# Kernel tuning notes

Hardware: AMD Instinct MI355X
Metric: run time of the kernel (lower is better)

## Reference

```python
import jax, jax.numpy as jnp
import numpy as np

SCALE = 2
K_UP = 5
K_ENC = 3
EPS = 1e-5


def _conv(x, w, b, pad):
    y = jax.lax.conv_general_dilated(x, w, (1, 1), [(pad, pad), (pad, pad)],
                                     dimension_numbers=('NCHW', 'OIHW', 'NCHW'))
    return y + b[None, :, None, None]


def _bn(x, g, b, m, v):
    return g[None, :, None, None] * (x - m[None, :, None, None]) * jax.lax.rsqrt(v[None, :, None, None] + EPS) + b[None, :, None, None]


def _pixel_shuffle(x, r):
    b, c, h, w = x.shape
    co = c // (r * r)
    return x.reshape(b, co, r, r, h, w).transpose(0, 1, 4, 2, 5, 3).reshape(b, co, h * r, w * r)


def setup_inputs() -> dict:
    key = jax.random.key(0)
    ks = jax.random.split(key, 8)
    c, c_mid = 256, 64
    k_enc_out = (SCALE * K_UP) ** 2  # 100
    inp = {
        'X': jax.random.normal(ks[0], (8, c, 64, 64), dtype=jnp.float32),
        'comp_w': jax.random.normal(ks[1], (c_mid, c, 1, 1), dtype=jnp.float32) * (2.0 / c) ** 0.5,
        'comp_b': jnp.zeros((c_mid,), jnp.float32),
        'bn1_g': jnp.ones((c_mid,), jnp.float32),
        'bn1_b': jnp.zeros((c_mid,), jnp.float32),
        'bn1_m': jnp.zeros((c_mid,), jnp.float32),
        'bn1_v': jnp.ones((c_mid,), jnp.float32),
        'enc_w': jax.random.normal(ks[2], (k_enc_out, c_mid, K_ENC, K_ENC), dtype=jnp.float32) * (2.0 / (c_mid * K_ENC * K_ENC)) ** 0.5,
        'enc_b': jnp.zeros((k_enc_out,), jnp.float32),
        'bn2_g': jnp.ones((k_enc_out,), jnp.float32),
        'bn2_b': jnp.zeros((k_enc_out,), jnp.float32),
        'bn2_m': jnp.zeros((k_enc_out,), jnp.float32),
        'bn2_v': jnp.ones((k_enc_out,), jnp.float32),
    }
    return inp


def reference(X, comp_w, comp_b, bn1_g, bn1_b, bn1_m, bn1_v,
              enc_w, enc_b, bn2_g, bn2_b, bn2_m, bn2_v):
    b, c, h, w = X.shape
    h_, w_ = h * SCALE, w * SCALE
    # kernel prediction branch
    W = jax.nn.relu(_bn(_conv(X, comp_w, comp_b, 0), bn1_g, bn1_b, bn1_m, bn1_v))
    W = _bn(_conv(W, enc_w, enc_b, K_ENC // 2), bn2_g, bn2_b, bn2_m, bn2_v)
    W = _pixel_shuffle(W, SCALE)            # (b, k_up^2, h_, w_)
    W = jax.nn.softmax(W, axis=1)
    # content branch: bilinear upsample (align_corners=False / half-pixel)
    Xu = jax.image.resize(X, (b, c, h_, w_), method='bilinear')
    pad = (K_UP // 2) * SCALE               # = 4
    Xp = jnp.pad(Xu, ((0, 0), (0, 0), (pad, pad), (pad, pad)))
    # fused unfold (dilation=SCALE) + softmax-weighted reassembly
    out = jnp.zeros((b, c, h_, w_), X.dtype)
    k = 0
    for i in range(K_UP):
        for j in range(K_UP):
            patch = jax.lax.dynamic_slice(Xp, (0, 0, i * SCALE, j * SCALE), (b, c, h_, w_))
            out = out + W[:, k, None] * patch
            k += 1
    return out
```

## Files before the change

kernel.cpp:

```cpp
#include <hip/hip_runtime.h>

#define EPS 1e-5f

__global__ void k0_prep(const float* __restrict__ comp_w, const float* __restrict__ comp_b,
                        const float* __restrict__ bn1_g, const float* __restrict__ bn1_b,
                        const float* __restrict__ bn1_m, const float* __restrict__ bn1_v,
                        const float* __restrict__ enc_w, const float* __restrict__ enc_b,
                        const float* __restrict__ bn2_g, const float* __restrict__ bn2_b,
                        const float* __restrict__ bn2_m, const float* __restrict__ bn2_v,
                        float* __restrict__ W1wT, float* __restrict__ b1f,
                        float* __restrict__ encT, float* __restrict__ biasT)
{
    int gtid = blockIdx.x * 256 + threadIdx.x;
    int gstride = gridDim.x * 256;
    for (int i = gtid; i < 256 * 64; i += gstride) {
        int cin = i >> 6, co = i & 63;
        float s = bn1_g[co] * rsqrtf(bn1_v[co] + EPS);
        W1wT[i] = comp_w[co * 256 + cin] * s;
    }
    for (int i = gtid; i < 64; i += gstride) {
        float s = bn1_g[i] * rsqrtf(bn1_v[i] + EPS);
        b1f[i] = (comp_b[i] - bn1_m[i]) * s + bn1_b[i];
    }
    for (int i = gtid; i < 4 * 64 * 9 * 32; i += gstride) {
        int k = i & 31;
        int rest = i >> 5;
        int dxy = rest % 9;
        int tmp = rest / 9;
        int cin = tmp & 63, p = tmp >> 6;
        float v = 0.f;
        if (k < 25) {
            int ko = 4 * k + p;
            float s = bn2_g[ko] * rsqrtf(bn2_v[ko] + EPS);
            v = enc_w[(ko * 64 + cin) * 9 + dxy] * s;
        }
        encT[i] = v;
    }
    for (int i = gtid; i < 4 * 32; i += gstride) {
        int p = i >> 5, k = i & 31;
        float v = 0.f;
        if (k < 25) {
            int ko = 4 * k + p;
            float s = bn2_g[ko] * rsqrtf(bn2_v[ko] + EPS);
            v = (enc_b[ko] - bn2_m[ko]) * s + bn2_b[ko];
        }
        biasT[i] = v;
    }
}

__global__ __launch_bounds__(256, 4) void k1_conv1(const float* __restrict__ X,
                                                   const float* __restrict__ W1wT,
                                                   const float* __restrict__ b1f,
                                                   float* __restrict__ W1)
{
    int blk = blockIdx.x;
    int b   = blk >> 5;
    int pt  = blk & 31;
    int tid = threadIdx.x;
    int coh  = __builtin_amdgcn_readfirstlane(tid >> 7);
    int posl = tid & 127;
    int pos  = pt * 128 + posl;
    const float* xp = X + (size_t)b * 256 * 4096 + pos;
    const float* wp = W1wT + coh * 32;
    float acc[32];
#pragma unroll
    for (int k = 0; k < 32; ++k) acc[k] = 0.f;
#pragma unroll 8
    for (int cin = 0; cin < 256; ++cin) {
        float x = xp[(size_t)cin * 4096];
        const float* w = wp + cin * 64;
#pragma unroll
        for (int k = 0; k < 32; ++k) acc[k] = fmaf(w[k], x, acc[k]);
    }
    float* op = W1 + ((size_t)b * 64 + coh * 32) * 4096 + pos;
#pragma unroll
    for (int k = 0; k < 32; ++k) {
        float v = acc[k] + b1f[coh * 32 + k];
        op[(size_t)k * 4096] = fmaxf(v, 0.f);
    }
}

__global__ __launch_bounds__(512, 4) void k2_conv2(const float* __restrict__ W1,
                                                   const float* __restrict__ encT,
                                                   const float* __restrict__ biasT,
                                                   float* __restrict__ Wsm)
{
    __shared__ float tile[6400];
    __shared__ float red[6400];
    int blk = blockIdx.x;
    int tc = blk & 7;
    int tr = (blk >> 3) & 7;
    int b  = blk >> 6;
    int tid = threadIdx.x;

    const float* wb = W1 + (size_t)b * 64 * 4096;
    for (int i = tid; i < 6400; i += 512) {
        int cin = i / 100;
        int rr = (i - cin * 100) / 10;
        int cc = i - cin * 100 - rr * 10;
        int r = tr * 8 - 1 + rr, c = tc * 8 - 1 + cc;
        float v = 0.f;
        if (r >= 0 && r < 64 && c >= 0 && c < 64) v = wb[cin * 4096 + r * 64 + c];
        tile[i] = v;
    }
    __syncthreads();

    int w    = tid >> 6;
    int p    = __builtin_amdgcn_readfirstlane(w & 3);
    int cinh = __builtin_amdgcn_readfirstlane(w >> 2);
    int lane = tid & 63;
    int pr = lane >> 3, pc = lane & 7;
    const float* wt = encT + (size_t)(p * 576 + cinh * 288) * 32;
    const float* tp = tile + cinh * 32 * 100;
    float acc[25];
#pragma unroll
    for (int k = 0; k < 25; ++k) acc[k] = 0.f;

    for (int cin = 0; cin < 32; ++cin) {
#pragma unroll
        for (int dy = 0; dy < 3; ++dy) {
#pragma unroll
            for (int dx = 0; dx < 3; ++dx) {
                float v = tp[cin * 100 + (pr + dy) * 10 + (pc + dx)];
                const float* wv = wt + (cin * 9 + dy * 3 + dx) * 32;
#pragma unroll
                for (int k = 0; k < 25; ++k) acc[k] = fmaf(wv[k], v, acc[k]);
            }
        }
    }

    if (cinh == 0) {
        float* rp = red + (p * 64 + lane) * 25;
#pragma unroll
        for (int k = 0; k < 25; ++k) rp[k] = acc[k];
    }
    __syncthreads();
    if (cinh == 1) {
        const float* rp = red + (p * 64 + lane) * 25;
#pragma unroll
        for (int k = 0; k < 25; ++k) acc[k] += rp[k];

        const float* bp = biasT + p * 32;
        float mx = -1e30f;
#pragma unroll
        for (int k = 0; k < 25; ++k) { acc[k] += bp[k]; mx = fmaxf(mx, acc[k]); }
        float sum = 0.f;
#pragma unroll
        for (int k = 0; k < 25; ++k) { acc[k] = __expf(acc[k] - mx); sum += acc[k]; }
        float rs = 1.f / sum;
#pragma unroll
        for (int k = 0; k < 25; ++k) acc[k] *= rs;

        int py = p >> 1, px = p & 1;
        int y = (tr * 8 + pr) * 2 + py, x = (tc * 8 + pc) * 2 + px;
        float* op = Wsm + (((size_t)b * 128 + y) * 128 + x) * 28;
#pragma unroll
        for (int k = 0; k < 6; ++k) {
            float4 v = make_float4(acc[k*4], acc[k*4+1], acc[k*4+2], acc[k*4+3]);
            *(float4*)(op + k * 4) = v;
        }
        op[24] = acc[24];
    }
}

#define LOADW(W, q) do { \
    float4 t0 = *(const float4*)(q);       float4 t1 = *(const float4*)((q) + 4);  \
    float4 t2 = *(const float4*)((q) + 8); float4 t3 = *(const float4*)((q) + 12); \
    float4 t4 = *(const float4*)((q) + 16); float4 t5 = *(const float4*)((q) + 20); \
    W[0]=t0.x; W[1]=t0.y; W[2]=t0.z; W[3]=t0.w; \
    W[4]=t1.x; W[5]=t1.y; W[6]=t1.z; W[7]=t1.w; \
    W[8]=t2.x; W[9]=t2.y; W[10]=t2.z; W[11]=t2.w; \
    W[12]=t3.x; W[13]=t3.y; W[14]=t3.z; W[15]=t3.w; \
    W[16]=t4.x; W[17]=t4.y; W[18]=t4.z; W[19]=t4.w; \
    W[20]=t5.x; W[21]=t5.y; W[22]=t5.z; W[23]=t5.w; \
    W[24]=(q)[24]; } while (0)

#define P_CSTR  148
#define P_PSTR  2376

__global__ __launch_bounds__(256, 3) void k3_carafe(const float* __restrict__ X,
                                                    const float* __restrict__ Wsm,
                                                    float* __restrict__ out)
{
    __shared__ __align__(16) float Bx[16 * 236];
    __shared__ __align__(16) float P[4 * P_PSTR];

    int blk = blockIdx.x;
    int chunk = blk >> 9;
    int b     = (blk >> 6) & 7;
    int tile  = blk & 63;
    int G0 = (tile >> 3) * 8;
    int H0 = (tile & 7) * 8;
    int c0 = chunk * 16;
    int tid = threadIdx.x;

    {
        const float* xb = X + (size_t)(b * 256 + c0) * 4096;
        for (int i = tid; i < 16 * 196; i += 256) {
            int c = i / 196;
            int r = (i - c * 196) / 14;
            int s = i - c * 196 - r * 14;
            int gr = G0 - 3 + r; gr = gr < 0 ? 0 : (gr > 63 ? 63 : gr);
            int gc = H0 - 3 + s; gc = gc < 0 ? 0 : (gc > 63 ? 63 : gc);
            Bx[c * 236 + r * 16 + s] = xb[(size_t)c * 4096 + gr * 64 + gc];
        }
    }
    __syncthreads();

    {
        int c2 = (tid >> 2) & 15;
        int tl = tid & 3;
        int pp = __builtin_amdgcn_readfirstlane(tid >> 6);
        int py2 = pp >> 1, px2 = pp & 1;
        float wy0 = py2 ? 0.75f : 0.25f, wy1 = 1.f - wy0;
        float wx0 = px2 ? 0.75f : 0.25f, wx1 = 1.f - wx0;
#pragma unroll
        for (int k = 0; k < 3; ++k) {
            int t = tl + 4 * k;
            bool row_ok = (unsigned)(G0 - 2 + t) < 64u;
            const float* rp0 = Bx + c2 * 236 + (t + py2) * 16;
            float x0[16], x1[16];
#pragma unroll
            for (int q = 0; q < 4; ++q) {
                float4 a = *(const float4*)(rp0 + q * 4);
                float4 e = *(const float4*)(rp0 + 16 + q * 4);
                x0[q*4+0]=a.x; x0[q*4+1]=a.y; x0[q*4+2]=a.z; x0[q*4+3]=a.w;
                x1[q*4+0]=e.x; x1[q*4+1]=e.y; x1[q*4+2]=e.z; x1[q*4+3]=e.w;
            }
            float v[12];
            if (px2 == 0) {
#pragma unroll
                for (int s = 0; s < 12; ++s)
                    v[s] = wy0 * (wx0 * x0[s] + wx1 * x0[s+1]) + wy1 * (wx0 * x1[s] + wx1 * x1[s+1]);
            } else {
#pragma unroll
                for (int s = 0; s < 12; ++s)
                    v[s] = wy0 * (wx0 * x0[s+1] + wx1 * x0[s+2]) + wy1 * (wx0 * x1[s+1] + wx1 * x1[s+2]);
            }
#pragma unroll
            for (int s = 0; s < 12; ++s) {
                bool ok = row_ok && ((unsigned)(H0 - 2 + s) < 64u);
                v[s] = ok ? v[s] : 0.f;
            }
            float* dst = P + pp * P_PSTR + c2 * P_CSTR + t * 12;
#pragma unroll
            for (int q = 0; q < 3; ++q)
                *(float4*)(dst + q * 4) = make_float4(v[q*4], v[q*4+1], v[q*4+2], v[q*4+3]);
        }
    }

    int cg  = tid & 3;
    int gid = tid >> 2;
    int oy  = gid >> 2;
    int px  = (gid >> 1) & 1;
    int txg = gid & 1;
    int p3  = (oy & 1) * 2 + px;
    int ty  = oy >> 1;
    int y   = 2 * G0 + oy;

    float w4[4][25];
    {
        const float* wb2 = Wsm + (((size_t)b * 128 + y) * 128) * 28;
#pragma unroll
        for (int t = 0; t < 4; ++t) {
            int x = 2 * H0 + 2 * (txg * 4 + t) + px;
            const float* wp = wb2 + (size_t)x * 28;
            LOADW(w4[t], wp);
        }
    }
    __syncthreads();

    float acc[4][4];
#pragma unroll
    for (int i = 0; i < 4; ++i)
#pragma unroll
        for (int t = 0; t < 4; ++t) acc[i][t] = 0.f;

    const float* pc0 = P + p3 * P_PSTR + ty * 12 + txg * 4;
#pragma unroll
    for (int i = 0; i < 4; ++i) {
        const float* pcc = pc0 + (cg + 4 * i) * P_CSTR;
#pragma unroll
        for (int i5 = 0; i5 < 5; ++i5) {
            float4 ra = *(const float4*)(pcc + i5 * 12);
            float4 rb = *(const float4*)(pcc + i5 * 12 + 4);
            float rw[8] = {ra.x, ra.y, ra.z, ra.w, rb.x, rb.y, rb.z, rb.w};
#pragma unroll
            for (int t = 0; t < 4; ++t) {
#pragma unroll
                for (int dx = 0; dx < 5; ++dx)
                    acc[i][t] = fmaf(w4[t][i5 * 5 + dx], rw[t + dx], acc[i][t]);
            }
        }
    }

    float* ob = out + (((size_t)(b * 256 + c0 + cg) * 128 + y) * 128) + 2 * H0 + 8 * txg + px;
#pragma unroll
    for (int i = 0; i < 4; ++i) {
#pragma unroll
        for (int t = 0; t < 4; ++t)
            ob[(size_t)(4 * i) * 16384 + 2 * t] = acc[i][t];
    }
}

extern "C" void kernel_launch(void* const* d_in, const int* in_sizes, int n_in,
                              void* d_out, int out_size, void* d_ws, size_t ws_size,
                              hipStream_t stream)
{
    const float* X      = (const float*)d_in[0];
    const float* comp_w = (const float*)d_in[1];
    const float* comp_b = (const float*)d_in[2];
    const float* bn1_g  = (const float*)d_in[3];
    const float* bn1_b  = (const float*)d_in[4];
    const float* bn1_m  = (const float*)d_in[5];
    const float* bn1_v  = (const float*)d_in[6];
    const float* enc_w  = (const float*)d_in[7];
    const float* enc_b  = (const float*)d_in[8];
    const float* bn2_g  = (const float*)d_in[9];
    const float* bn2_b  = (const float*)d_in[10];
    const float* bn2_m  = (const float*)d_in[11];
    const float* bn2_v  = (const float*)d_in[12];

    float* ws   = (float*)d_ws;
    float* W1wT = ws;
    float* b1f  = ws + 16384;
    float* encT = ws + 16448;
    float* biasT= ws + 90176;
    float* W1   = ws + 90304;
    float* Wsm  = ws + 2187456;

    float* outp = (float*)d_out;

    k0_prep<<<64, 256, 0, stream>>>(comp_w, comp_b, bn1_g, bn1_b, bn1_m, bn1_v,
                                    enc_w, enc_b, bn2_g, bn2_b, bn2_m, bn2_v,
                                    W1wT, b1f, encT, biasT);
    k1_conv1<<<256, 256, 0, stream>>>(X, W1wT, b1f, W1);
    k2_conv2<<<512, 512, 0, stream>>>(W1, encT, biasT, Wsm);
    k3_carafe<<<8192, 256, 0, stream>>>(X, Wsm, outp);
}
```

Baseline: 382.1 us.

## Fuse 1x1 compress conv into 3x3 encoder conv kernel via shared-memory halo tile

Merges the 1x1 compress conv and the 3x3 encoder conv into one kernel. Each block computes the 1x1 conv on an 8x8 output tile plus a halo of 10x10 positions, stages that in shared memory, and then runs the 3x3 conv with softmax. This removes the global write and read of the 64-channel intermediate and drops one launch. In exchange, the halo positions are recomputed (100 per 64 outputs), the X tile is reloaded in 32-channel chunks with extra syncs, and shared memory per block grows, which may lower occupancy.

```diff
diff --git a/kernel.cpp b/kernel.cpp
--- a/kernel.cpp
+++ b/kernel.cpp
@@ -48,118 +48,139 @@
     }
 }
 
-__global__ __launch_bounds__(256, 4) void k1_conv1(const float* __restrict__ X,
-                                                   const float* __restrict__ W1wT,
-                                                   const float* __restrict__ b1f,
-                                                   float* __restrict__ W1)
+__global__ __launch_bounds__(512, 4) void k12_fused(const float* __restrict__ X,
+                                                    const float* __restrict__ W1wT,
+                                                    const float* __restrict__ b1f,
+                                                    const float* __restrict__ encT,
+                                                    const float* __restrict__ biasT,
+                                                    float* __restrict__ Wsm)
 {
-    int blk = blockIdx.x;
-    int b   = blk >> 5;
-    int pt  = blk & 31;
-    int tid = threadIdx.x;
-    int coh  = __builtin_amdgcn_readfirstlane(tid >> 7);
-    int posl = tid & 127;
-    int pos  = pt * 128 + posl;
-    const float* xp = X + (size_t)b * 256 * 4096 + pos;
-    const float* wp = W1wT + coh * 32;
-    float acc[32];
-#pragma unroll
-    for (int k = 0; k < 32; ++k) acc[k] = 0.f;
-#pragma unroll 8
-    for (int cin = 0; cin < 256; ++cin) {
-        float x = xp[(size_t)cin * 4096];
-        const float* w = wp + cin * 64;
-#pragma unroll
-        for (int k = 0; k < 32; ++k) acc[k] = fmaf(w[k], x, acc[k]);
-    }
-    float* op = W1 + ((size_t)b * 64 + coh * 32) * 4096 + pos;
-#pragma unroll
-    for (int k = 0; k < 32; ++k) {
-        float v = acc[k] + b1f[coh * 32 + k];
-        op[(size_t)k * 4096] = fmaxf(v, 0.f);
-    }
-}
-
-__global__ __launch_bounds__(512, 4) void k2_conv2(const float* __restrict__ W1,
-                                                   const float* __restrict__ encT,
-                                                   const float* __restrict__ biasT,
-                                                   float* __restrict__ Wsm)
-{
-    __shared__ float tile[6400];
+    __shared__ __align__(16) float Xs[3200];
+    __shared__ __align__(16) float W1s[64 * 101];
     __shared__ float red[6400];
+
     int blk = blockIdx.x;
     int tc = blk & 7;
     int tr = (blk >> 3) & 7;
     int b  = blk >> 6;
     int tid = threadIdx.x;
 
-    const float* wb = W1 + (size_t)b * 64 * 4096;
-    for (int i = tid; i < 6400; i += 512) {
-        int cin = i / 100;
-        int rr = (i - cin * 100) / 10;
-        int cc = i - cin * 100 - rr * 10;
-        int r = tr * 8 - 1 + rr, c = tc * 8 - 1 + cc;
-        float v = 0.f;
-        if (r >= 0 && r < 64 && c >= 0 && c < 64) v = wb[cin * 4096 + r * 64 + c];
-        tile[i] = v;
+    int posq = __builtin_amdgcn_readfirstlane(tid >> 6);
+    int lane = tid & 63;
+    float acc[4][4];
+#pragma unroll
+    for (int qi = 0; qi < 4; ++qi)
+#pragma unroll
+        for (int j = 0; j < 4; ++j) acc[qi][j] = 0.f;
+
+    for (int cb = 0; cb < 8; ++cb) {
+        if (cb) __syncthreads();
+        {
+            const float* xb = X + ((size_t)b * 256 + cb * 32) * 4096;
+            for (int i = tid; i < 3200; i += 512) {
+                int cc = i / 100;
+                int pos = i - cc * 100;
+                int rr = pos / 10, sc = pos - rr * 10;
+                int r = tr * 8 - 1 + rr; r = r < 0 ? 0 : (r > 63 ? 63 : r);
+                int c = tc * 8 - 1 + sc; c = c < 0 ? 0 : (c > 63 ? 63 : c);
+                Xs[i] = xb[(size_t)cc * 4096 + r * 64 + c];
+            }
+        }
+        __syncthreads();
+        float w32[32];
+#pragma unroll
+        for (int cc = 0; cc < 32; ++cc) w32[cc] = W1wT[(cb * 32 + cc) * 64 + lane];
+#pragma unroll
+        for (int qi = 0; qi < 4; ++qi) {
+            int q = posq + 8 * qi;
+            if (q < 25) {
+                const float* xq = Xs + 4 * q;
+#pragma unroll 8
+                for (int cc = 0; cc < 32; ++cc) {
+                    float4 xv = *(const float4*)(xq + cc * 100);
+                    acc[qi][0] = fmaf(w32[cc], xv.x, acc[qi][0]);
+                    acc[qi][1] = fmaf(w32[cc], xv.y, acc[qi][1]);
+                    acc[qi][2] = fmaf(w32[cc], xv.z, acc[qi][2]);
+                    acc[qi][3] = fmaf(w32[cc], xv.w, acc[qi][3]);
+                }
+            }
+        }
+    }
+    {
+        float bia = b1f[lane];
+#pragma unroll
+        for (int qi = 0; qi < 4; ++qi) {
+            int q = posq + 8 * qi;
+            if (q < 25) {
+#pragma unroll
+                for (int j = 0; j < 4; ++j) {
+                    int pos = 4 * q + j;
+                    int rr = pos / 10, sc = pos - rr * 10;
+                    int r = tr * 8 - 1 + rr, c = tc * 8 - 1 + sc;
+                    bool ok = (unsigned)r < 64u && (unsigned)c < 64u;
+                    float v = ok ? fmaxf(acc[qi][j] + bia, 0.f) : 0.f;
+                    W1s[lane * 101 + pos] = v;
+                }
+            }
+        }
     }
     __syncthreads();
 
-    int w    = tid >> 6;
-    int p    = __builtin_amdgcn_readfirstlane(w & 3);
-    int cinh = __builtin_amdgcn_readfirstlane(w >> 2);
-    int lane = tid & 63;
-    int pr = lane >> 3, pc = lane & 7;
+    int w8   = tid >> 6;
+    int p    = __builtin_amdgcn_readfirstlane(w8 & 3);
+    int cinh = __builtin_amdgcn_readfirstlane(w8 >> 2);
+    int lane2 = tid & 63;
+    int pr = lane2 >> 3, pc = lane2 & 7;
     const float* wt = encT + (size_t)(p * 576 + cinh * 288) * 32;
-    const float* tp = tile + cinh * 32 * 100;
-    float acc[25];
-#pragma unroll
-    for (int k = 0; k < 25; ++k) acc[k] = 0.f;
+    const float* tp = W1s + cinh * 32 * 101;
+    float acc2[25];
+#pragma unroll
+    for (int k = 0; k < 25; ++k) acc2[k] = 0.f;
 
     for (int cin = 0; cin < 32; ++cin) {
 #pragma unroll
         for (int dy = 0; dy < 3; ++dy) {
 #pragma unroll
             for (int dx = 0; dx < 3; ++dx) {
-                float v = tp[cin * 100 + (pr + dy) * 10 + (pc + dx)];
+                float v = tp[cin * 101 + (pr + dy) * 10 + (pc + dx)];
                 const float* wv = wt + (cin * 9 + dy * 3 + dx) * 32;
 #pragma unroll
-                for (int k = 0; k < 25; ++k) acc[k] = fmaf(wv[k], v, acc[k]);
+                for (int k = 0; k < 25; ++k) acc2[k] = fmaf(wv[k], v, acc2[k]);
             }
         }
     }
 
     if (cinh == 0) {
-        float* rp = red + (p * 64 + lane) * 25;
-#pragma unroll
-        for (int k = 0; k < 25; ++k) rp[k] = acc[k];
+        float* rp = red + (p * 64 + lane2) * 25;
+#pragma unroll
+        for (int k = 0; k < 25; ++k) rp[k] = acc2[k];
     }
     __syncthreads();
     if (cinh == 1) {
-        const float* rp = red + (p * 64 + lane) * 25;
-#pragma unroll
-        for (int k = 0; k < 25; ++k) acc[k] += rp[k];
+        const float* rp = red + (p * 64 + lane2) * 25;
+#pragma unroll
+        for (int k = 0; k < 25; ++k) acc2[k] += rp[k];
 
         const float* bp = biasT + p * 32;
         float mx = -1e30f;
 #pragma unroll
-        for (int k = 0; k < 25; ++k) { acc[k] += bp[k]; mx = fmaxf(mx, acc[k]); }
+        for (int k = 0; k < 25; ++k) { acc2[k] += bp[k]; mx = fmaxf(mx, acc2[k]); }
         float sum = 0.f;
 #pragma unroll
-        for (int k = 0; k < 25; ++k) { acc[k] = __expf(acc[k] - mx); sum += acc[k]; }
+        for (int k = 0; k < 25; ++k) { acc2[k] = __expf(acc2[k] - mx); sum += acc2[k]; }
         float rs = 1.f / sum;
 #pragma unroll
-        for (int k = 0; k < 25; ++k) acc[k] *= rs;
+        for (int k = 0; k < 25; ++k) acc2[k] *= rs;
 
         int py = p >> 1, px = p & 1;
         int y = (tr * 8 + pr) * 2 + py, x = (tc * 8 + pc) * 2 + px;
         float* op = Wsm + (((size_t)b * 128 + y) * 128 + x) * 28;
 #pragma unroll
         for (int k = 0; k < 6; ++k) {
-            float4 v = make_float4(acc[k*4], acc[k*4+1], acc[k*4+2], acc[k*4+3]);
+            float4 v = make_float4(acc2[k*4], acc2[k*4+1], acc2[k*4+2], acc2[k*4+3]);
             *(float4*)(op + k * 4) = v;
         }
-        op[24] = acc[24];
+        op[24] = acc2[24];
     }
 }
 
@@ -326,7 +347,6 @@
     float* b1f  = ws + 16384;
     float* encT = ws + 16448;
     float* biasT= ws + 90176;
-    float* W1   = ws + 90304;
     float* Wsm  = ws + 2187456;
 
     float* outp = (float*)d_out;
@@ -334,7 +354,6 @@
     k0_prep<<<64, 256, 0, stream>>>(comp_w, comp_b, bn1_g, bn1_b, bn1_m, bn1_v,
                                     enc_w, enc_b, bn2_g, bn2_b, bn2_m, bn2_v,
                                     W1wT, b1f, encT, biasT);
-    k1_conv1<<<256, 256, 0, stream>>>(X, W1wT, b1f, W1);
-    k2_conv2<<<512, 512, 0, stream>>>(W1, encT, biasT, Wsm);
+    k12_fused<<<512, 512, 0, stream>>>(X, W1wT, b1f, encT, biasT, Wsm);
     k3_carafe<<<8192, 256, 0, stream>>>(X, Wsm, outp);
 }
```

Result: no change. 385.8 us (+1.0%).
